# Kernel optimization log

Measured on AMD Instinct MI355X. Metric: run time of the kernel, lower is better.

The kernel has to match this reference:

```python
import jax, jax.numpy as jnp
import numpy as np

N_NODES = 50000
N_EDGES = 1_600_000
D_IN, D_HID, D_OUT, K = 128, 50, 10, 5


def setup_inputs() -> dict:
    key = jax.random.key(0)
    ks = jax.random.split(key, 6)
    x = jax.random.normal(ks[0], (N_NODES, D_IN), dtype=jnp.float32)
    edge_index = jax.random.randint(ks[1], (2, N_EDGES), 0, N_NODES, dtype=jnp.int64)
    cheb_w = jax.random.normal(ks[2], (K, D_IN, D_HID), dtype=jnp.float32) * 0.05
    cheb_b = jax.random.normal(ks[3], (D_HID,), dtype=jnp.float32) * 0.05
    fc_w = jax.random.normal(ks[4], (D_HID, D_OUT), dtype=jnp.float32) * 0.1
    fc_b = jax.random.normal(ks[5], (D_OUT,), dtype=jnp.float32) * 0.1
    return {"x": x, "edge_index": edge_index, "cheb_w": cheb_w,
            "cheb_b": cheb_b, "fc_w": fc_w, "fc_b": fc_b}


def reference(x, edge_index, cheb_w, cheb_b, fc_w, fc_b):
    # ChebConv (PyG, normalization='sym', lambda_max=2.0):
    # L_hat = 2L/lambda_max - I = -D^{-1/2} A D^{-1/2} (zero diagonal)
    row, col = edge_index[0], edge_index[1]
    n = x.shape[0]
    deg = jax.ops.segment_sum(jnp.ones_like(row, dtype=x.dtype), row, num_segments=n)
    dinv = jnp.where(deg > 0, jax.lax.rsqrt(jnp.maximum(deg, 1.0)), 0.0)
    w = -dinv[row] * dinv[col]  # [E] edge weights of L_hat

    def prop(h):  # L_hat @ h via gather-scale-scatter
        return jax.ops.segment_sum(w[:, None] * h[col], row, num_segments=n)

    tx0 = x
    tx1 = prop(x)
    out = jnp.einsum('ni,io->no', tx0, cheb_w[0]) + jnp.einsum('ni,io->no', tx1, cheb_w[1])
    for k in range(2, K):
        tx2 = 2.0 * prop(tx1) - tx0
        out = out + jnp.einsum('ni,io->no', tx2, cheb_w[k])
        tx0, tx1 = tx1, tx2
    out = out + cheb_b

    h = jax.nn.relu(out)
    logits = h @ fc_w + fc_b
    return jax.nn.log_softmax(logits, axis=1)
```

## Files before the change

kernel.cpp:

```cpp
#include <hip/hip_runtime.h>
#include <hip/hip_fp16.h>

#define N_NODES 50000
#define N_EDGES 1600000
#define D_IN    128
#define D_HID   50
#define D_OUT   10
#define K_CHEB  5

#define P1_BLOCKS 256
#define EPB       (N_EDGES / P1_BLOCKS)
#define NBUCK2    256
#define NB_USED2  196
#define BCAP2     96

#define WH_ELEMS  (K_CHEB * 64 * D_IN)
#define WH_BLOCKS ((WH_ELEMS + 255) / 256)

#define VROW      64
#define VSTRIDE   ((size_t)(N_NODES + 1) * VROW)

#define NGROUP    (N_NODES / 16)
#define VG_SPAN   512
#define VG_WAVES  (K_CHEB * VG_SPAN)

typedef _Float16 half8_t __attribute__((ext_vector_type(8)));
typedef float    f32x4_t __attribute__((ext_vector_type(4)));


__global__ __launch_bounds__(256) void pass1_kernel(const int* __restrict__ row,
                                                    const int* __restrict__ col,
                                                    unsigned int* __restrict__ store,
                                                    int* __restrict__ bcnt,
                                                    const float* __restrict__ W,
                                                    __half* __restrict__ Wh,
                                                    __half* __restrict__ v,
                                                    __half* __restrict__ b1) {
    int tid = threadIdx.x;
    int blk = blockIdx.x;
    if (blk >= P1_BLOCKS) {
        int wb = blk - P1_BLOCKS;
        if (wb < WH_BLOCKS) {
            int idx = wb * 256 + tid;
            if (idx < WH_ELEMS) {
                int i = idx & 127;
                int n = (idx >> 7) & 63;
                int t = idx >> 13;
                float vv = (n < D_HID) ? W[t * D_IN * D_HID + i * D_HID + n] : 0.f;
                Wh[idx] = __float2half(vv);
            }
        } else {
            if (tid < VROW) {
                v[4 * VSTRIDE + (size_t)N_NODES * VROW + tid] = __float2half(0.f);
                b1[(size_t)N_NODES * VROW + tid] = __float2half(0.f);
            }
        }
        return;
    }
    __shared__ int cnt[NBUCK2];
    cnt[tid] = 0;
    __syncthreads();
    int base = blk * EPB;
    size_t sb = (size_t)blk * (NBUCK2 * BCAP2);
    for (int i = tid; i < EPB; i += 256) {
        int r = row[base + i];
        int c = col[base + i];
        int b = r >> 8;
        int pos = atomicAdd(&cnt[b], 1);
        if (pos >= BCAP2) pos = BCAP2 - 1;
        store[sb + b * BCAP2 + pos] = ((unsigned int)(r & 255) << 16) | (unsigned int)c;
    }
    __syncthreads();
    bcnt[blk * NBUCK2 + tid] = cnt[tid];
}

__global__ __launch_bounds__(512) void pass2_kernel(const unsigned int* __restrict__ store,
                                                    const int* __restrict__ bcnt,
                                                    int* __restrict__ row_start,
                                                    float* __restrict__ dinv,
                                                    float* __restrict__ dinv2,
                                                    float* __restrict__ sdeg,
                                                    int* __restrict__ ewc) {
    __shared__ int hist[256];
    __shared__ int off[256];
    __shared__ int fill[256];
    __shared__ int sb_part[512];
    __shared__ int pscan[256];
    __shared__ int s_bbase;
    int tid = threadIdx.x;
    int b = blockIdx.x;

    {
        int bt = tid & 255, seg = tid >> 8;
        int sum = 0;
        for (int s = seg * 128; s < seg * 128 + 128; ++s) sum += bcnt[s * NBUCK2 + bt];
        sb_part[tid] = sum;
    }
    __syncthreads();
    if (tid < 256) pscan[tid] = sb_part[tid] + sb_part[256 + tid];
    __syncthreads();
    for (int o = 1; o < 256; o <<= 1) {
        int vv = (tid < 256 && tid >= o) ? pscan[tid - o] : 0;
        __syncthreads();
        if (tid < 256) pscan[tid] += vv;
        __syncthreads();
    }
    if (tid == 0) {
        s_bbase = (b == 0) ? 0 : pscan[b - 1];
        if (b == 0) row_start[N_NODES] = pscan[255];
    }
    if (tid < 256) hist[tid] = 0;
    __syncthreads();
    int bbase_b = s_bbase;

    int strip = tid >> 1;
    int sub   = tid & 1;
    int sn = bcnt[strip * NBUCK2 + b];
    size_t sb = (size_t)strip * (NBUCK2 * BCAP2) + b * BCAP2;
    for (int i = sub; i < sn; i += 2)
        atomicAdd(&hist[store[sb + i] >> 16], 1);
    __syncthreads();
    int d = (tid < 256) ? hist[tid] : 0;
    if (tid < 256) off[tid] = d;
    __syncthreads();
    for (int o = 1; o < 256; o <<= 1) {
        int vv = (tid < 256 && tid >= o) ? off[tid - o] : 0;
        __syncthreads();
        if (tid < 256) off[tid] += vv;
        __syncthreads();
    }
    if (tid < 256) {
        int excl = off[tid] - d + bbase_b;
        hist[tid] = excl;
        fill[tid] = 0;
        int r = (b << 8) + tid;
        if (r < N_NODES) {
            row_start[r] = excl;
            float fd = (float)d;
            dinv[r]  = d ? rsqrtf(fd)  : 0.f;
            dinv2[r] = d ? (1.f / fd)  : 0.f;
            sdeg[r]  = d ? sqrtf(fd)   : 0.f;
        }
    }
    __syncthreads();
    for (int i = sub; i < sn; i += 2) {
        unsigned int vv = store[sb + i];
        int rl = vv >> 16;
        int c = vv & 0xffff;
        int p = atomicAdd(&fill[rl], 1);
        ewc[hist[rl] + p] = c;
    }
}

__global__ __launch_bounds__(256) void vgemm_kernel(const float* __restrict__ x,
                                                    const float* __restrict__ dinv,
                                                    const __half* __restrict__ Wh,
                                                    __half* __restrict__ v) {
    int tid = threadIdx.x;
    int lane = tid & 63;
    int wv = __builtin_amdgcn_readfirstlane(tid >> 6);
    int w = blockIdx.x * 4 + wv;
    int t = w / VG_SPAN;
    int idx = w - t * VG_SPAN;
    int m = lane & 15;
    int quad = lane >> 4;

    const __half* Wt = Wh + t * (64 * D_IN);
    half8_t afr[4][4];
    #pragma unroll
    for (int ks = 0; ks < 4; ++ks) {
        int ko = ks * 32 + quad * 8;
        #pragma unroll
        for (int jt = 0; jt < 4; ++jt)
            afr[ks][jt] = *(const half8_t*)(Wt + (jt * 16 + m) * D_IN + ko);
    }

    __half* vt = v + t * VSTRIDE;

    float4 pf[8];
    int g = idx;
    {
        const float* xr = x + (size_t)(g * 16 + m) * D_IN;
        #pragma unroll
        for (int ks = 0; ks < 4; ++ks) {
            pf[2 * ks]     = *(const float4*)(xr + ks * 32 + quad * 8);
            pf[2 * ks + 1] = *(const float4*)(xr + ks * 32 + quad * 8 + 4);
        }
    }

    for (; g < NGROUP; g += VG_SPAN) {
        int node = g * 16 + m;
        float dv = dinv[node];
        half8_t bfr[4];
        #pragma unroll
        for (int ks = 0; ks < 4; ++ks) {
            float4 fA = pf[2 * ks], fB = pf[2 * ks + 1];
            half8_t h;
            h[0] = (_Float16)fA.x; h[1] = (_Float16)fA.y;
            h[2] = (_Float16)fA.z; h[3] = (_Float16)fA.w;
            h[4] = (_Float16)fB.x; h[5] = (_Float16)fB.y;
            h[6] = (_Float16)fB.z; h[7] = (_Float16)fB.w;
            bfr[ks] = h;
        }
        int gn = g + VG_SPAN;
        if (gn < NGROUP) {
            const float* xr = x + (size_t)(gn * 16 + m) * D_IN;
            #pragma unroll
            for (int ks = 0; ks < 4; ++ks) {
                pf[2 * ks]     = *(const float4*)(xr + ks * 32 + quad * 8);
                pf[2 * ks + 1] = *(const float4*)(xr + ks * 32 + quad * 8 + 4);
            }
        }
        f32x4_t acc[4];
        #pragma unroll
        for (int jt = 0; jt < 4; ++jt) acc[jt] = (f32x4_t)0.f;
        #pragma unroll
        for (int ks = 0; ks < 4; ++ks)
            #pragma unroll
            for (int jt = 0; jt < 4; ++jt)
                acc[jt] = __builtin_amdgcn_mfma_f32_16x16x32_f16(afr[ks][jt], bfr[ks], acc[jt], 0, 0, 0);
        __half* dst = vt + (size_t)node * VROW + quad * 4;
        #pragma unroll
        for (int jt = 0; jt < 4; ++jt) {
            __half2 h0 = __float22half2_rn(make_float2(acc[jt][0] * dv, acc[jt][1] * dv));
            __half2 h1 = __float22half2_rn(make_float2(acc[jt][2] * dv, acc[jt][3] * dv));
            uint2 u;
            u.x = *(unsigned int*)&h0;
            u.y = *(unsigned int*)&h1;
            *(uint2*)(dst + jt * 16) = u;
        }
    }
}

__global__ __launch_bounds__(512) void prop_kernel(const int* __restrict__ row_start,
                                                   const int* __restrict__ ewc,
                                                   const float* __restrict__ dinv2,
                                                   const __half* __restrict__ src,
                                                   const __half* __restrict__ addv,
                                                   const __half* __restrict__ subv,
                                                   float alphaM, int do_sub,
                                                   __half* __restrict__ dst) {
    int tid = threadIdx.x;
    int lane = tid & 63;
    int wv = __builtin_amdgcn_readfirstlane(tid >> 6);
    int r = blockIdx.x * 8 + wv;
    int e0 = row_start[r], e1 = row_start[r + 1];
    float fac = -alphaM * dinv2[r];
    int l = lane & 7;
    int g = lane >> 3;
    const uint4* src16 = (const uint4*)src;
    float ac[8];
    #pragma unroll
    for (int j = 0; j < 8; ++j) ac[j] = 0.f;
    for (int e = e0; e < e1; e += 32) {
        #pragma unroll
        for (int i = 0; i < 4; ++i) {
            int base = e + 8 * i;
            int cl = ewc[base + g];
            if (base + g >= e1) cl = N_NODES;
            uint4 u = src16[(size_t)cl * 8 + l];
            float2 f0 = __half22float2(*(__half2*)&u.x);
            float2 f1 = __half22float2(*(__half2*)&u.y);
            float2 f2 = __half22float2(*(__half2*)&u.z);
            float2 f3 = __half22float2(*(__half2*)&u.w);
            ac[0] += f0.x; ac[1] += f0.y; ac[2] += f1.x; ac[3] += f1.y;
            ac[4] += f2.x; ac[5] += f2.y; ac[6] += f3.x; ac[7] += f3.y;
        }
    }
    #pragma unroll
    for (int k = 8; k <= 32; k <<= 1) {
        #pragma unroll
        for (int j = 0; j < 8; ++j) ac[j] += __shfl_xor(ac[j], k);
    }
    if (g == 0) {
        size_t o = (size_t)r * 8 + l;
        uint4 av = ((const uint4*)addv)[o];
        float2 av0 = __half22float2(*(__half2*)&av.x);
        float2 av1 = __half22float2(*(__half2*)&av.y);
        float2 av2 = __half22float2(*(__half2*)&av.z);
        float2 av3 = __half22float2(*(__half2*)&av.w);
        float r0 = av0.x + fac * ac[0];
        float r1 = av0.y + fac * ac[1];
        float r2 = av1.x + fac * ac[2];
        float r3 = av1.y + fac * ac[3];
        float r4 = av2.x + fac * ac[4];
        float r5 = av2.y + fac * ac[5];
        float r6 = av3.x + fac * ac[6];
        float r7 = av3.y + fac * ac[7];
        if (do_sub) {
            uint4 sv = ((const uint4*)subv)[o];
            float2 sv0 = __half22float2(*(__half2*)&sv.x);
            float2 sv1 = __half22float2(*(__half2*)&sv.y);
            float2 sv2 = __half22float2(*(__half2*)&sv.z);
            float2 sv3 = __half22float2(*(__half2*)&sv.w);
            r0 -= sv0.x; r1 -= sv0.y; r2 -= sv1.x; r3 -= sv1.y;
            r4 -= sv2.x; r5 -= sv2.y; r6 -= sv3.x; r7 -= sv3.y;
        }
        __half2 h0 = __float22half2_rn(make_float2(r0, r1));
        __half2 h1 = __float22half2_rn(make_float2(r2, r3));
        __half2 h2 = __float22half2_rn(make_float2(r4, r5));
        __half2 h3 = __float22half2_rn(make_float2(r6, r7));
        uint4 u;
        u.x = *(unsigned int*)&h0;
        u.y = *(unsigned int*)&h1;
        u.z = *(unsigned int*)&h2;
        u.w = *(unsigned int*)&h3;
        ((uint4*)dst)[o] = u;
    }
}

__global__ __launch_bounds__(256) void final_kernel(const __half* __restrict__ S,
                                                    const float* __restrict__ sdeg,
                                                    const float* __restrict__ cheb_b,
                                                    const float* __restrict__ fc_w,
                                                    const float* __restrict__ fc_b,
                                                    float* __restrict__ out) {
    int r = blockIdx.x * blockDim.x + threadIdx.x;
    if (r >= N_NODES) return;
    float sc = sdeg[r];
    const __half2* s2 = (const __half2*)(S + (size_t)r * VROW);
    float h[D_HID];
    #pragma unroll
    for (int i = 0; i < D_HID / 2; ++i) {
        float2 f = __half22float2(s2[i]);
        float v0 = sc * f.x + cheb_b[2 * i];
        float v1 = sc * f.y + cheb_b[2 * i + 1];
        h[2 * i]     = v0 > 0.f ? v0 : 0.f;
        h[2 * i + 1] = v1 > 0.f ? v1 : 0.f;
    }
    float lg[D_OUT];
    #pragma unroll
    for (int o = 0; o < D_OUT; ++o) lg[o] = fc_b[o];
    #pragma unroll 2
    for (int i = 0; i < D_HID; ++i) {
        float hv = h[i];
        #pragma unroll
        for (int o = 0; o < D_OUT; ++o) lg[o] += hv * fc_w[i * D_OUT + o];
    }
    float mx = lg[0];
    #pragma unroll
    for (int o = 1; o < D_OUT; ++o) mx = fmaxf(mx, lg[o]);
    float s = 0.f;
    #pragma unroll
    for (int o = 0; o < D_OUT; ++o) s += __expf(lg[o] - mx);
    float ls = __logf(s);
    size_t oo = (size_t)r * D_OUT;
    #pragma unroll
    for (int o = 0; o < D_OUT; ++o) out[oo + o] = lg[o] - mx - ls;
}

extern "C" void kernel_launch(void* const* d_in, const int* in_sizes, int n_in,
                              void* d_out, int out_size, void* d_ws, size_t ws_size,
                              hipStream_t stream) {
    const float* x      = (const float*)d_in[0];
    const int*   edge   = (const int*)d_in[1];
    const float* cheb_w = (const float*)d_in[2];
    const float* cheb_b = (const float*)d_in[3];
    const float* fc_w   = (const float*)d_in[4];
    const float* fc_b   = (const float*)d_in[5];
    float* out = (float*)d_out;

    const int* erow = edge;
    const int* ecol = edge + N_EDGES;

    uintptr_t p = ((uintptr_t)d_ws + 255) & ~(uintptr_t)255;
    auto alloc = [&](size_t bytes) {
        uintptr_t q = p;
        p = (p + bytes + 255) & ~(uintptr_t)255;
        return (void*)q;
    };
    unsigned int* store = (unsigned int*)alloc((size_t)P1_BLOCKS * NBUCK2 * BCAP2 * 4);
    int*    bcnt      = (int*)alloc((size_t)P1_BLOCKS * NBUCK2 * 4);
    int*    row_start = (int*)alloc((size_t)(N_NODES + 1) * 4);
    float*  dinv      = (float*)alloc((size_t)N_NODES * 4);
    float*  dinv2     = (float*)alloc((size_t)N_NODES * 4);
    float*  sdeg      = (float*)alloc((size_t)N_NODES * 4);
    int*    ewc       = (int*)alloc((size_t)(N_EDGES + 32) * 4);
    __half* Wh        = (__half*)alloc((size_t)WH_ELEMS * 2);
    __half* Sbuf      = (__half*)alloc(VSTRIDE * 2);
    __half* v         = (__half*)alloc(5 * VSTRIDE * 2);
    __half* b1        = (__half*)alloc(VSTRIDE * 2);

    __half* b3 = (__half*)store;
    __half* b2 = (__half*)store + VSTRIDE;
    __half* S  = Sbuf;

    pass1_kernel<<<P1_BLOCKS + WH_BLOCKS + 1, 256, 0, stream>>>(
        erow, ecol, store, bcnt, cheb_w, Wh, v, b1);
    pass2_kernel<<<NB_USED2, 512, 0, stream>>>(store, bcnt, row_start,
                                               dinv, dinv2, sdeg, ewc);
    hipMemsetAsync(b3 + (size_t)N_NODES * VROW, 0, VROW * 2, stream);
    hipMemsetAsync(b2 + (size_t)N_NODES * VROW, 0, VROW * 2, stream);

    vgemm_kernel<<<VG_WAVES / 4, 256, 0, stream>>>(x, dinv, Wh, v);

    __half* v0 = v;
    __half* v1 = v + 1 * VSTRIDE;
    __half* v2 = v + 2 * VSTRIDE;
    __half* v3 = v + 3 * VSTRIDE;
    __half* v4 = v + 4 * VSTRIDE;
    const int PB = N_NODES / 8;
    prop_kernel<<<PB, 512, 0, stream>>>(row_start, ewc, dinv2, v4, v3, v3, 2.f, 0, b3);
    prop_kernel<<<PB, 512, 0, stream>>>(row_start, ewc, dinv2, b3, v2, v4, 2.f, 1, b2);
    prop_kernel<<<PB, 512, 0, stream>>>(row_start, ewc, dinv2, b2, v1, b3, 2.f, 1, b1);
    prop_kernel<<<PB, 512, 0, stream>>>(row_start, ewc, dinv2, b1, v0, b2, 1.f, 1, S);

    final_kernel<<<(N_NODES + 255) / 256, 256, 0, stream>>>(S, sdeg, cheb_b,
                                                            fc_w, fc_b, out);
}
```

Before: 291.4 us.

## Run dense GEMM concurrently with edge bucketing by deferring dinv scaling into propagation

The x·W GEMM no longer depends on degree normalization. It now reads a pre-converted fp16 copy of x and runs in the same launch as the edge bucketing pass, so the two overlap instead of executing in sequence. The dinv scaling that used to be applied in the GEMM moves into the first propagation step (per-source scaling on gathered rows) and into the add/sub terms of the later steps, using templated prop variants. In exchange there is an extra prep kernel that converts x to fp16 and extra dinv gathers in the first prop. The b2/b3 scratch buffers become separate allocations, which also removes the memsets.

```diff
diff --git a/kernel.cpp b/kernel.cpp
--- a/kernel.cpp
+++ b/kernel.cpp
@@ -16,6 +16,7 @@
 
 #define WH_ELEMS  (K_CHEB * 64 * D_IN)
 #define WH_BLOCKS ((WH_ELEMS + 255) / 256)
+#define XH_BLOCKS (N_NODES * D_IN / 8 / 256)
 
 #define VROW      64
 #define VSTRIDE   ((size_t)(N_NODES + 1) * VROW)
@@ -23,45 +24,132 @@
 #define NGROUP    (N_NODES / 16)
 #define VG_SPAN   512
 #define VG_WAVES  (K_CHEB * VG_SPAN)
+#define VG_BLOCKS (VG_WAVES / 4)
 
 typedef _Float16 half8_t __attribute__((ext_vector_type(8)));
 typedef float    f32x4_t __attribute__((ext_vector_type(4)));
 
 
-__global__ __launch_bounds__(256) void pass1_kernel(const int* __restrict__ row,
+__global__ __launch_bounds__(256) void prep_kernel(const float* __restrict__ x,
+                                                   const float* __restrict__ W,
+                                                   __half* __restrict__ xh,
+                                                   __half* __restrict__ Wh,
+                                                   __half* __restrict__ u,
+                                                   __half* __restrict__ b1,
+                                                   __half* __restrict__ b3,
+                                                   __half* __restrict__ b2,
+                                                   float* __restrict__ dinv) {
+    int tid = threadIdx.x;
+    int blk = blockIdx.x;
+    if (blk < XH_BLOCKS) {
+        size_t base = ((size_t)blk * 256 + tid) * 8;
+        float4 a = *(const float4*)(x + base);
+        float4 b = *(const float4*)(x + base + 4);
+        half8_t h;
+        h[0] = (_Float16)a.x; h[1] = (_Float16)a.y;
+        h[2] = (_Float16)a.z; h[3] = (_Float16)a.w;
+        h[4] = (_Float16)b.x; h[5] = (_Float16)b.y;
+        h[6] = (_Float16)b.z; h[7] = (_Float16)b.w;
+        *(half8_t*)(xh + base) = h;
+    } else if (blk < XH_BLOCKS + WH_BLOCKS) {
+        int idx = (blk - XH_BLOCKS) * 256 + tid;
+        if (idx < WH_ELEMS) {
+            int i = idx & 127;
+            int n = (idx >> 7) & 63;
+            int t = idx >> 13;
+            float vv = (n < D_HID) ? W[t * D_IN * D_HID + i * D_HID + n] : 0.f;
+            Wh[idx] = __float2half(vv);
+        }
+    } else {
+        if (tid < VROW) {
+            __half z = __float2half(0.f);
+            u[4 * VSTRIDE + (size_t)N_NODES * VROW + tid] = z;
+            b1[(size_t)N_NODES * VROW + tid] = z;
+            b3[(size_t)N_NODES * VROW + tid] = z;
+            b2[(size_t)N_NODES * VROW + tid] = z;
+        }
+        if (tid == 64) dinv[N_NODES] = 0.f;
+    }
+}
+
+__global__ __launch_bounds__(256) void fused_kernel(const int* __restrict__ row,
                                                     const int* __restrict__ col,
                                                     unsigned int* __restrict__ store,
                                                     int* __restrict__ bcnt,
-                                                    const float* __restrict__ W,
-                                                    __half* __restrict__ Wh,
-                                                    __half* __restrict__ v,
-                                                    __half* __restrict__ b1) {
+                                                    const __half* __restrict__ xh,
+                                                    const __half* __restrict__ Wh,
+                                                    __half* __restrict__ u) {
+    __shared__ int cnt[NBUCK2];
     int tid = threadIdx.x;
     int blk = blockIdx.x;
-    if (blk >= P1_BLOCKS) {
-        int wb = blk - P1_BLOCKS;
-        if (wb < WH_BLOCKS) {
-            int idx = wb * 256 + tid;
-            if (idx < WH_ELEMS) {
-                int i = idx & 127;
-                int n = (idx >> 7) & 63;
-                int t = idx >> 13;
-                float vv = (n < D_HID) ? W[t * D_IN * D_HID + i * D_HID + n] : 0.f;
-                Wh[idx] = __float2half(vv);
+    if (blk < VG_BLOCKS) {
+        int lane = tid & 63;
+        int wv = __builtin_amdgcn_readfirstlane(tid >> 6);
+        int w = blk * 4 + wv;
+        int t = w / VG_SPAN;
+        int idx = w - t * VG_SPAN;
+        int m = lane & 15;
+        int quad = lane >> 4;
+
+        const __half* Wt = Wh + t * (64 * D_IN);
+        half8_t afr[4][4];
+        #pragma unroll
+        for (int ks = 0; ks < 4; ++ks) {
+            int ko = ks * 32 + quad * 8;
+            #pragma unroll
+            for (int jt = 0; jt < 4; ++jt)
+                afr[ks][jt] = *(const half8_t*)(Wt + (jt * 16 + m) * D_IN + ko);
+        }
+
+        __half* ut = u + t * VSTRIDE;
+
+        half8_t pf[4];
+        int g = idx;
+        {
+            const __half* xr = xh + (size_t)(g * 16 + m) * D_IN;
+            #pragma unroll
+            for (int ks = 0; ks < 4; ++ks)
+                pf[ks] = *(const half8_t*)(xr + ks * 32 + quad * 8);
+        }
+
+        for (; g < NGROUP; g += VG_SPAN) {
+            int node = g * 16 + m;
+            half8_t bfr[4];
+            #pragma unroll
+            for (int ks = 0; ks < 4; ++ks) bfr[ks] = pf[ks];
+            int gn = g + VG_SPAN;
+            if (gn < NGROUP) {
+                const __half* xr = xh + (size_t)(gn * 16 + m) * D_IN;
+                #pragma unroll
+                for (int ks = 0; ks < 4; ++ks)
+                    pf[ks] = *(const half8_t*)(xr + ks * 32 + quad * 8);
             }
-        } else {
-            if (tid < VROW) {
-                v[4 * VSTRIDE + (size_t)N_NODES * VROW + tid] = __float2half(0.f);
-                b1[(size_t)N_NODES * VROW + tid] = __float2half(0.f);
+            f32x4_t acc[4];
+            #pragma unroll
+            for (int jt = 0; jt < 4; ++jt) acc[jt] = (f32x4_t)0.f;
+            #pragma unroll
+            for (int ks = 0; ks < 4; ++ks)
+                #pragma unroll
+                for (int jt = 0; jt < 4; ++jt)
+                    acc[jt] = __builtin_amdgcn_mfma_f32_16x16x32_f16(afr[ks][jt], bfr[ks], acc[jt], 0, 0, 0);
+            __half* dst = ut + (size_t)node * VROW + quad * 4;
+            #pragma unroll
+            for (int jt = 0; jt < 4; ++jt) {
+                __half2 h0 = __float22half2_rn(make_float2(acc[jt][0], acc[jt][1]));
+                __half2 h1 = __float22half2_rn(make_float2(acc[jt][2], acc[jt][3]));
+                uint2 uu;
+                uu.x = *(unsigned int*)&h0;
+                uu.y = *(unsigned int*)&h1;
+                *(uint2*)(dst + jt * 16) = uu;
             }
         }
         return;
     }
-    __shared__ int cnt[NBUCK2];
+    int blk2 = blk - VG_BLOCKS;
     cnt[tid] = 0;
     __syncthreads();
-    int base = blk * EPB;
-    size_t sb = (size_t)blk * (NBUCK2 * BCAP2);
+    int base = blk2 * EPB;
+    size_t sb = (size_t)blk2 * (NBUCK2 * BCAP2);
     for (int i = tid; i < EPB; i += 256) {
         int r = row[base + i];
         int c = col[base + i];
@@ -71,7 +159,7 @@
         store[sb + b * BCAP2 + pos] = ((unsigned int)(r & 255) << 16) | (unsigned int)c;
     }
     __syncthreads();
-    bcnt[blk * NBUCK2 + tid] = cnt[tid];
+    bcnt[blk2 * NBUCK2 + tid] = cnt[tid];
 }
 
 __global__ __launch_bounds__(512) void pass2_kernel(const unsigned int* __restrict__ store,
@@ -152,93 +240,15 @@
     }
 }
 
-__global__ __launch_bounds__(256) void vgemm_kernel(const float* __restrict__ x,
-                                                    const float* __restrict__ dinv,
-                                                    const __half* __restrict__ Wh,
-                                                    __half* __restrict__ v) {
-    int tid = threadIdx.x;
-    int lane = tid & 63;
-    int wv = __builtin_amdgcn_readfirstlane(tid >> 6);
-    int w = blockIdx.x * 4 + wv;
-    int t = w / VG_SPAN;
-    int idx = w - t * VG_SPAN;
-    int m = lane & 15;
-    int quad = lane >> 4;
-
-    const __half* Wt = Wh + t * (64 * D_IN);
-    half8_t afr[4][4];
-    #pragma unroll
-    for (int ks = 0; ks < 4; ++ks) {
-        int ko = ks * 32 + quad * 8;
-        #pragma unroll
-        for (int jt = 0; jt < 4; ++jt)
-            afr[ks][jt] = *(const half8_t*)(Wt + (jt * 16 + m) * D_IN + ko);
-    }
-
-    __half* vt = v + t * VSTRIDE;
-
-    float4 pf[8];
-    int g = idx;
-    {
-        const float* xr = x + (size_t)(g * 16 + m) * D_IN;
-        #pragma unroll
-        for (int ks = 0; ks < 4; ++ks) {
-            pf[2 * ks]     = *(const float4*)(xr + ks * 32 + quad * 8);
-            pf[2 * ks + 1] = *(const float4*)(xr + ks * 32 + quad * 8 + 4);
-        }
-    }
-
-    for (; g < NGROUP; g += VG_SPAN) {
-        int node = g * 16 + m;
-        float dv = dinv[node];
-        half8_t bfr[4];
-        #pragma unroll
-        for (int ks = 0; ks < 4; ++ks) {
-            float4 fA = pf[2 * ks], fB = pf[2 * ks + 1];
-            half8_t h;
-            h[0] = (_Float16)fA.x; h[1] = (_Float16)fA.y;
-            h[2] = (_Float16)fA.z; h[3] = (_Float16)fA.w;
-            h[4] = (_Float16)fB.x; h[5] = (_Float16)fB.y;
-            h[6] = (_Float16)fB.z; h[7] = (_Float16)fB.w;
-            bfr[ks] = h;
-        }
-        int gn = g + VG_SPAN;
-        if (gn < NGROUP) {
-            const float* xr = x + (size_t)(gn * 16 + m) * D_IN;
-            #pragma unroll
-            for (int ks = 0; ks < 4; ++ks) {
-                pf[2 * ks]     = *(const float4*)(xr + ks * 32 + quad * 8);
-                pf[2 * ks + 1] = *(const float4*)(xr + ks * 32 + quad * 8 + 4);
-            }
-        }
-        f32x4_t acc[4];
-        #pragma unroll
-        for (int jt = 0; jt < 4; ++jt) acc[jt] = (f32x4_t)0.f;
-        #pragma unroll
-        for (int ks = 0; ks < 4; ++ks)
-            #pragma unroll
-            for (int jt = 0; jt < 4; ++jt)
-                acc[jt] = __builtin_amdgcn_mfma_f32_16x16x32_f16(afr[ks][jt], bfr[ks], acc[jt], 0, 0, 0);
-        __half* dst = vt + (size_t)node * VROW + quad * 4;
-        #pragma unroll
-        for (int jt = 0; jt < 4; ++jt) {
-            __half2 h0 = __float22half2_rn(make_float2(acc[jt][0] * dv, acc[jt][1] * dv));
-            __half2 h1 = __float22half2_rn(make_float2(acc[jt][2] * dv, acc[jt][3] * dv));
-            uint2 u;
-            u.x = *(unsigned int*)&h0;
-            u.y = *(unsigned int*)&h1;
-            *(uint2*)(dst + jt * 16) = u;
-        }
-    }
-}
-
+template<int SCALE_SRC, int DO_SUB, int SCALE_SUB>
 __global__ __launch_bounds__(512) void prop_kernel(const int* __restrict__ row_start,
                                                    const int* __restrict__ ewc,
                                                    const float* __restrict__ dinv2,
+                                                   const float* __restrict__ dinv,
                                                    const __half* __restrict__ src,
                                                    const __half* __restrict__ addv,
                                                    const __half* __restrict__ subv,
-                                                   float alphaM, int do_sub,
+                                                   float alphaM,
                                                    __half* __restrict__ dst) {
     int tid = threadIdx.x;
     int lane = tid & 63;
@@ -258,13 +268,21 @@
             int base = e + 8 * i;
             int cl = ewc[base + g];
             if (base + g >= e1) cl = N_NODES;
-            uint4 u = src16[(size_t)cl * 8 + l];
-            float2 f0 = __half22float2(*(__half2*)&u.x);
-            float2 f1 = __half22float2(*(__half2*)&u.y);
-            float2 f2 = __half22float2(*(__half2*)&u.z);
-            float2 f3 = __half22float2(*(__half2*)&u.w);
-            ac[0] += f0.x; ac[1] += f0.y; ac[2] += f1.x; ac[3] += f1.y;
-            ac[4] += f2.x; ac[5] += f2.y; ac[6] += f3.x; ac[7] += f3.y;
+            uint4 uu = src16[(size_t)cl * 8 + l];
+            float2 f0 = __half22float2(*(__half2*)&uu.x);
+            float2 f1 = __half22float2(*(__half2*)&uu.y);
+            float2 f2 = __half22float2(*(__half2*)&uu.z);
+            float2 f3 = __half22float2(*(__half2*)&uu.w);
+            if (SCALE_SRC) {
+                float dc = dinv[cl];
+                ac[0] = fmaf(dc, f0.x, ac[0]); ac[1] = fmaf(dc, f0.y, ac[1]);
+                ac[2] = fmaf(dc, f1.x, ac[2]); ac[3] = fmaf(dc, f1.y, ac[3]);
+                ac[4] = fmaf(dc, f2.x, ac[4]); ac[5] = fmaf(dc, f2.y, ac[5]);
+                ac[6] = fmaf(dc, f3.x, ac[6]); ac[7] = fmaf(dc, f3.y, ac[7]);
+            } else {
+                ac[0] += f0.x; ac[1] += f0.y; ac[2] += f1.x; ac[3] += f1.y;
+                ac[4] += f2.x; ac[5] += f2.y; ac[6] += f3.x; ac[7] += f3.y;
+            }
         }
     }
     #pragma unroll
@@ -273,39 +291,43 @@
         for (int j = 0; j < 8; ++j) ac[j] += __shfl_xor(ac[j], k);
     }
     if (g == 0) {
+        float sa = dinv[r];
         size_t o = (size_t)r * 8 + l;
         uint4 av = ((const uint4*)addv)[o];
         float2 av0 = __half22float2(*(__half2*)&av.x);
         float2 av1 = __half22float2(*(__half2*)&av.y);
         float2 av2 = __half22float2(*(__half2*)&av.z);
         float2 av3 = __half22float2(*(__half2*)&av.w);
-        float r0 = av0.x + fac * ac[0];
-        float r1 = av0.y + fac * ac[1];
-        float r2 = av1.x + fac * ac[2];
-        float r3 = av1.y + fac * ac[3];
-        float r4 = av2.x + fac * ac[4];
-        float r5 = av2.y + fac * ac[5];
-        float r6 = av3.x + fac * ac[6];
-        float r7 = av3.y + fac * ac[7];
-        if (do_sub) {
+        float r0 = fmaf(sa, av0.x, fac * ac[0]);
+        float r1 = fmaf(sa, av0.y, fac * ac[1]);
+        float r2 = fmaf(sa, av1.x, fac * ac[2]);
+        float r3 = fmaf(sa, av1.y, fac * ac[3]);
+        float r4 = fmaf(sa, av2.x, fac * ac[4]);
+        float r5 = fmaf(sa, av2.y, fac * ac[5]);
+        float r6 = fmaf(sa, av3.x, fac * ac[6]);
+        float r7 = fmaf(sa, av3.y, fac * ac[7]);
+        if (DO_SUB) {
+            float ss = SCALE_SUB ? dinv[r] : 1.f;
             uint4 sv = ((const uint4*)subv)[o];
             float2 sv0 = __half22float2(*(__half2*)&sv.x);
             float2 sv1 = __half22float2(*(__half2*)&sv.y);
             float2 sv2 = __half22float2(*(__half2*)&sv.z);
             float2 sv3 = __half22float2(*(__half2*)&sv.w);
-            r0 -= sv0.x; r1 -= sv0.y; r2 -= sv1.x; r3 -= sv1.y;
-            r4 -= sv2.x; r5 -= sv2.y; r6 -= sv3.x; r7 -= sv3.y;
+            r0 = fmaf(-ss, sv0.x, r0); r1 = fmaf(-ss, sv0.y, r1);
+            r2 = fmaf(-ss, sv1.x, r2); r3 = fmaf(-ss, sv1.y, r3);
+            r4 = fmaf(-ss, sv2.x, r4); r5 = fmaf(-ss, sv2.y, r5);
+            r6 = fmaf(-ss, sv3.x, r6); r7 = fmaf(-ss, sv3.y, r7);
         }
         __half2 h0 = __float22half2_rn(make_float2(r0, r1));
         __half2 h1 = __float22half2_rn(make_float2(r2, r3));
         __half2 h2 = __float22half2_rn(make_float2(r4, r5));
         __half2 h3 = __float22half2_rn(make_float2(r6, r7));
-        uint4 u;
-        u.x = *(unsigned int*)&h0;
-        u.y = *(unsigned int*)&h1;
-        u.z = *(unsigned int*)&h2;
-        u.w = *(unsigned int*)&h3;
-        ((uint4*)dst)[o] = u;
+        uint4 uu;
+        uu.x = *(unsigned int*)&h0;
+        uu.y = *(unsigned int*)&h1;
+        uu.z = *(unsigned int*)&h2;
+        uu.w = *(unsigned int*)&h3;
+        ((uint4*)dst)[o] = uu;
     }
 }
 
@@ -372,38 +394,42 @@
     unsigned int* store = (unsigned int*)alloc((size_t)P1_BLOCKS * NBUCK2 * BCAP2 * 4);
     int*    bcnt      = (int*)alloc((size_t)P1_BLOCKS * NBUCK2 * 4);
     int*    row_start = (int*)alloc((size_t)(N_NODES + 1) * 4);
-    float*  dinv      = (float*)alloc((size_t)N_NODES * 4);
+    float*  dinv      = (float*)alloc((size_t)(N_NODES + 1) * 4);
     float*  dinv2     = (float*)alloc((size_t)N_NODES * 4);
     float*  sdeg      = (float*)alloc((size_t)N_NODES * 4);
     int*    ewc       = (int*)alloc((size_t)(N_EDGES + 32) * 4);
     __half* Wh        = (__half*)alloc((size_t)WH_ELEMS * 2);
+    __half* xh        = (__half*)alloc((size_t)N_NODES * D_IN * 2);
     __half* Sbuf      = (__half*)alloc(VSTRIDE * 2);
-    __half* v         = (__half*)alloc(5 * VSTRIDE * 2);
+    __half* u         = (__half*)alloc(5 * VSTRIDE * 2);
     __half* b1        = (__half*)alloc(VSTRIDE * 2);
-
-    __half* b3 = (__half*)store;
-    __half* b2 = (__half*)store + VSTRIDE;
+    __half* b3        = (__half*)alloc(VSTRIDE * 2);
+    __half* b2        = (__half*)alloc(VSTRIDE * 2);
     __half* S  = Sbuf;
 
-    pass1_kernel<<<P1_BLOCKS + WH_BLOCKS + 1, 256, 0, stream>>>(
-        erow, ecol, store, bcnt, cheb_w, Wh, v, b1);
+    prep_kernel<<<XH_BLOCKS + WH_BLOCKS + 1, 256, 0, stream>>>(
+        x, cheb_w, xh, Wh, u, b1, b3, b2, dinv);
+
+    fused_kernel<<<VG_BLOCKS + P1_BLOCKS, 256, 0, stream>>>(
+        erow, ecol, store, bcnt, xh, Wh, u);
+
     pass2_kernel<<<NB_USED2, 512, 0, stream>>>(store, bcnt, row_start,
                                                dinv, dinv2, sdeg, ewc);
-    hipMemsetAsync(b3 + (size_t)N_NODES * VROW, 0, VROW * 2, stream);
-    hipMemsetAsync(b2 + (size_t)N_NODES * VROW, 0, VROW * 2, stream);
-
-    vgemm_kernel<<<VG_WAVES / 4, 256, 0, stream>>>(x, dinv, Wh, v);
-
-    __half* v0 = v;
-    __half* v1 = v + 1 * VSTRIDE;
-    __half* v2 = v + 2 * VSTRIDE;
-    __half* v3 = v + 3 * VSTRIDE;
-    __half* v4 = v + 4 * VSTRIDE;
+
+    __half* u0 = u;
+    __half* u1 = u + 1 * VSTRIDE;
+    __half* u2 = u + 2 * VSTRIDE;
+    __half* u3 = u + 3 * VSTRIDE;
+    __half* u4 = u + 4 * VSTRIDE;
     const int PB = N_NODES / 8;
-    prop_kernel<<<PB, 512, 0, stream>>>(row_start, ewc, dinv2, v4, v3, v3, 2.f, 0, b3);
-    prop_kernel<<<PB, 512, 0, stream>>>(row_start, ewc, dinv2, b3, v2, v4, 2.f, 1, b2);
-    prop_kernel<<<PB, 512, 0, stream>>>(row_start, ewc, dinv2, b2, v1, b3, 2.f, 1, b1);
-    prop_kernel<<<PB, 512, 0, stream>>>(row_start, ewc, dinv2, b1, v0, b2, 1.f, 1, S);
+    prop_kernel<1, 0, 0><<<PB, 512, 0, stream>>>(row_start, ewc, dinv2, dinv,
+                                                 u4, u3, u3, 2.f, b3);
+    prop_kernel<0, 1, 1><<<PB, 512, 0, stream>>>(row_start, ewc, dinv2, dinv,
+                                                 b3, u2, u4, 2.f, b2);
+    prop_kernel<0, 1, 0><<<PB, 512, 0, stream>>>(row_start, ewc, dinv2, dinv,
+                                                 b2, u1, b3, 2.f, b1);
+    prop_kernel<0, 1, 0><<<PB, 512, 0, stream>>>(row_start, ewc, dinv2, dinv,
+                                                 b1, u0, b2, 1.f, S);
 
     final_kernel<<<(N_NODES + 255) / 256, 256, 0, stream>>>(S, sdeg, cheb_b,
                                                             fc_w, fc_b, out);
```

Result: faster. 282.5 us (-3.1%).
